# Kernel tuning notes

Measured on AMD Instinct MI355X. Metric: run time of the kernel, lower is better.

The kernel has to match this reference:

```python
import jax, jax.numpy as jnp
import numpy as np
from math import ceil, log2

LEVELS = 8
# pywt 'db4' filters (length 8)
DB4_DEC_HI = np.array([-0.23037781330885523, 0.7148465705525415, -0.6308807679295904,
                       -0.02798376941698385, 0.18703481171888114, 0.030841381835986965,
                       -0.032883011666982945, -0.010597401784997278], dtype=np.float32)
DB4_REC_HI = np.array([-0.010597401784997278, -0.032883011666982945, 0.030841381835986965,
                       0.18703481171888114, -0.02798376941698385, -0.6308807679295904,
                       0.7148465705525415, -0.23037781330885523], dtype=np.float32)


def setup_inputs() -> dict:
    key = jax.random.key(0)
    x = jax.random.normal(key, (2048, 3000), dtype=jnp.float32)
    scaling = jnp.tile(jnp.asarray(DB4_DEC_HI), (LEVELS, 1))       # [levels, 8]
    scaling_rec = jnp.tile(jnp.asarray(DB4_REC_HI), (LEVELS, 1))   # [levels, 8]
    return {"input": x, "scaling": scaling, "scaling_rec": scaling_rec}


def _make_wavelet(h):
    # g = flip(h); g[1::2] *= -1
    g = jnp.flip(h, axis=-1)
    signs = jnp.where(jnp.arange(g.shape[-1]) % 2 == 1, -1.0, 1.0).astype(g.dtype)
    return g * signs


def _circ_conv(x, filt, transpose=False):
    # FFT-based circular convolution (filter zero-padded to input length)
    L = x.shape[-1]
    ra = jnp.fft.rfft(x)
    rb = jnp.fft.rfft(filt, n=L)
    if transpose:
        rb = jnp.conj(rb)
    return jnp.fft.irfft(ra * rb, n=L)


def _upsample2(x):
    # interleave zeros: out[:, ::2] = x
    n, k = x.shape
    out = jnp.zeros((n, 2 * k), dtype=x.dtype)
    return out.at[:, ::2].set(x)


def _forward(x, scaling, scaling_rec):
    levels = scaling.shape[0]
    m = x.shape[1]
    L = 2 ** ceil(log2(m))
    p0 = (L - m) // 2
    p1 = ceil((L - m) / 2)
    x = jnp.pad(x, ((0, 0), (p0, p1)), mode="edge")  # ReplicationPad1d

    approx = x
    wav_coeffs = []
    for lvl in range(levels):
        wavelet = _make_wavelet(scaling_rec[lvl])
        details = _circ_conv(approx, wavelet)[:, ::2]
        approx = _circ_conv(approx, scaling[lvl])[:, ::2]
        wav_coeffs.append(details)
    wav_coeffs.append(approx)

    # (no thresholding: the original forward copies coeffs unmodified)
    filtered = list(wav_coeffs)
    approx = filtered[-1]
    for lvl in reversed(range(levels)):
        details = filtered[lvl]
        wav_syn = _make_wavelet(scaling_rec[lvl])
        d_rec = _circ_conv(_upsample2(details), wav_syn, transpose=True)
        a_rec = _circ_conv(_upsample2(approx), scaling[lvl], transpose=True)
        approx = d_rec + a_rec

    recon = approx[:, p0:m + p1]
    coeffs = jnp.concatenate(wav_coeffs, axis=-1)  # total length == L
    return recon, coeffs


def reference(input, scaling, scaling_rec):
    return _forward(input, scaling, scaling_rec)
```

## Files before the change

kernel.cpp:

```cpp
#include <hip/hip_runtime.h>

#define NROWS 2048
#define MLEN  3000
#define LPAD  4096
#define PAD0  548
#define NLVL  8
#define NT    256

__global__ __launch_bounds__(NT) void despawn_kernel(
    const float* __restrict__ x,
    const float* __restrict__ scaling,
    const float* __restrict__ scaling_rec,
    float* __restrict__ recon_out,
    float* __restrict__ coef_out)
{
    __shared__ float bufA[LPAD];
    __shared__ float bufB[LPAD / 2];
    __shared__ float coef[LPAD];
    __shared__ float fsca[NLVL * 8];
    __shared__ float fwav[NLVL * 8];

    const int tid = threadIdx.x;
    const int row = blockIdx.x;

    if (tid < NLVL * 8) {
        const int lvl = tid >> 3, k = tid & 7;
        fsca[tid] = scaling[tid];
        fwav[tid] = scaling_rec[lvl * 8 + (7 - k)] * ((k & 1) ? -1.0f : 1.0f);
    }

    const float* xr = x + (size_t)row * MLEN;
    for (int i = tid; i < LPAD; i += NT) {
        int j = i - PAD0;
        j = j < 0 ? 0 : (j > MLEN - 1 ? MLEN - 1 : j);
        bufA[i] = xr[j];
    }
    __syncthreads();

    float* cur = bufA;
    float* alt = bufB;
    int   Ml  = LPAD;
    int   coff = 0;
    for (int lvl = 0; lvl < NLVL; ++lvl) {
        const int half = Ml >> 1;
        const int mask = Ml - 1;
        const float* w = &fwav[lvl * 8];
        const float* s = &fsca[lvl * 8];
        for (int j = tid; j < half; j += NT) {
            const int b = 2 * j;
            float ds = 0.0f, as = 0.0f;
#pragma unroll
            for (int k = 0; k < 8; ++k) {
                const float v = cur[(b - k) & mask];
                ds = fmaf(v, w[k], ds);
                as = fmaf(v, s[k], as);
            }
            coef[coff + j] = ds;
            alt[j] = as;
        }
        __syncthreads();
        coff += half;
        float* t = cur; cur = alt; alt = t;
        Ml = half;
    }
    if (tid < 16) coef[LPAD - 16 + tid] = cur[tid];
    __syncthreads();

    const float* a = &coef[LPAD - 16];
    int len = 16;
    float* obuf = bufB;
    for (int lvl = NLVL - 1; lvl >= 0; --lvl) {
        const int Mout  = len << 1;
        const int lmask = len - 1;
        const float* d = &coef[LPAD - (LPAD >> lvl)];
        const float* w = &fwav[lvl * 8];
        const float* s = &fsca[lvl * 8];
        for (int n = tid; n < Mout; n += NT) {
            const int p = n & 1;
            float sum = 0.0f;
#pragma unroll
            for (int t4 = 0; t4 < 4; ++t4) {
                const int k   = p + 2 * t4;
                const int idx = ((n + k) >> 1) & lmask;
                sum = fmaf(d[idx], w[k], sum);
                sum = fmaf(a[idx], s[k], sum);
            }
            obuf[n] = sum;
        }
        __syncthreads();
        a   = obuf;
        len = Mout;
        obuf = (obuf == bufB) ? bufA : bufB;
    }

    float* ro = recon_out + (size_t)row * MLEN;
    for (int i = tid; i < MLEN; i += NT) ro[i] = a[PAD0 + i];

    float* co = coef_out + (size_t)row * LPAD;
    for (int i = tid; i < LPAD; i += NT) co[i] = coef[i];
}

extern "C" void kernel_launch(void* const* d_in, const int* in_sizes, int n_in,
                              void* d_out, int out_size, void* d_ws, size_t ws_size,
                              hipStream_t stream) {
    const float* x           = (const float*)d_in[0];
    const float* scaling     = (const float*)d_in[1];
    const float* scaling_rec = (const float*)d_in[2];
    float* recon = (float*)d_out;
    float* coefo = recon + (size_t)NROWS * MLEN;
    despawn_kernel<<<dim3(NROWS), dim3(NT), 0, stream>>>(x, scaling, scaling_rec,
                                                         recon, coefo);
    (void)in_sizes; (void)n_in; (void)out_size; (void)d_ws; (void)ws_size;
}
```

Measured before the change: 110.9 us.

## Store levels deinterleaved in LDS, keep detail coefficients in global memory, shrink LDS

The signal is kept in LDS split into even and odd halves, so the strided filter taps become contiguous reads and bank conflicts drop. Detail coefficients are written straight to the global output row and read back from there during reconstruction, instead of being staged in a 16 KB shared array. This removes the final LDS-to-global copy and cuts LDS per block from about 40 KB to about 24 KB, which allows more blocks per CU. The cost is that reconstruction reads details from global memory (L2-resident), and it relies on the block's own global writes being visible after __syncthreads.

After: 113.8 us. 2.6% more time.

```diff
diff --git a/kernel.cpp b/kernel.cpp
--- a/kernel.cpp
+++ b/kernel.cpp
@@ -14,14 +14,14 @@
     float* __restrict__ recon_out,
     float* __restrict__ coef_out)
 {
-    __shared__ float bufA[LPAD];
-    __shared__ float bufB[LPAD / 2];
-    __shared__ float coef[LPAD];
+    __shared__ float SA[LPAD];
+    __shared__ float SB[LPAD / 2];
     __shared__ float fsca[NLVL * 8];
     __shared__ float fwav[NLVL * 8];
 
     const int tid = threadIdx.x;
     const int row = blockIdx.x;
+    float* const crow = coef_out + (size_t)row * LPAD;
 
     if (tid < NLVL * 8) {
         const int lvl = tid >> 3, k = tid & 7;
@@ -33,71 +33,76 @@
     for (int i = tid; i < LPAD; i += NT) {
         int j = i - PAD0;
         j = j < 0 ? 0 : (j > MLEN - 1 ? MLEN - 1 : j);
-        bufA[i] = xr[j];
+        SA[((i & 1) ? (LPAD / 2) : 0) + (i >> 1)] = xr[j];
     }
     __syncthreads();
 
-    float* cur = bufA;
-    float* alt = bufB;
-    int   Ml  = LPAD;
-    int   coff = 0;
+    float* cur = SA;
+    float* alt = SB;
+    int M = LPAD;
+    int coff = 0;
     for (int lvl = 0; lvl < NLVL; ++lvl) {
-        const int half = Ml >> 1;
-        const int mask = Ml - 1;
-        const float* w = &fwav[lvl * 8];
-        const float* s = &fsca[lvl * 8];
-        for (int j = tid; j < half; j += NT) {
-            const int b = 2 * j;
+        const int H = M >> 1;
+        const int hm = H - 1;
+        const float* we = &fwav[lvl * 8];
+        const float* se = &fsca[lvl * 8];
+        const float* ev = cur;
+        const float* od = cur + H;
+        for (int j = tid; j < H; j += NT) {
             float ds = 0.0f, as = 0.0f;
 #pragma unroll
-            for (int k = 0; k < 8; ++k) {
-                const float v = cur[(b - k) & mask];
-                ds = fmaf(v, w[k], ds);
-                as = fmaf(v, s[k], as);
+            for (int m = 0; m < 4; ++m) {
+                const float vE = ev[(j - m) & hm];
+                const float vO = od[(j - m - 1) & hm];
+                ds = fmaf(vE, we[2 * m], ds);
+                ds = fmaf(vO, we[2 * m + 1], ds);
+                as = fmaf(vE, se[2 * m], as);
+                as = fmaf(vO, se[2 * m + 1], as);
             }
-            coef[coff + j] = ds;
-            alt[j] = as;
+            crow[coff + j] = ds;
+            alt[((j & 1) ? (H >> 1) : 0) + (j >> 1)] = as;
         }
         __syncthreads();
-        coff += half;
+        coff += H;
         float* t = cur; cur = alt; alt = t;
-        Ml = half;
+        M = H;
     }
-    if (tid < 16) coef[LPAD - 16 + tid] = cur[tid];
+    if (tid < 16) {
+        const float v = cur[((tid & 1) ? 8 : 0) + (tid >> 1)];
+        crow[LPAD - 16 + tid] = v;
+        SA[16 + tid] = v;
+    }
     __syncthreads();
 
-    const float* a = &coef[LPAD - 16];
+    const float* a = SA + 16;
     int len = 16;
-    float* obuf = bufB;
+    float* obuf = SB;
     for (int lvl = NLVL - 1; lvl >= 0; --lvl) {
-        const int Mout  = len << 1;
+        const int Mout = len << 1;
         const int lmask = len - 1;
-        const float* d = &coef[LPAD - (LPAD >> lvl)];
-        const float* w = &fwav[lvl * 8];
-        const float* s = &fsca[lvl * 8];
+        const float* d = crow + (LPAD - (LPAD >> lvl));
+        const float* we = &fwav[lvl * 8];
+        const float* se = &fsca[lvl * 8];
         for (int n = tid; n < Mout; n += NT) {
             const int p = n & 1;
+            const int i0 = (n + p) >> 1;
             float sum = 0.0f;
 #pragma unroll
-            for (int t4 = 0; t4 < 4; ++t4) {
-                const int k   = p + 2 * t4;
-                const int idx = ((n + k) >> 1) & lmask;
-                sum = fmaf(d[idx], w[k], sum);
-                sum = fmaf(a[idx], s[k], sum);
+            for (int m = 0; m < 4; ++m) {
+                const int idx = (i0 + m) & lmask;
+                sum = fmaf(d[idx], we[p + 2 * m], sum);
+                sum = fmaf(a[idx], se[p + 2 * m], sum);
             }
             obuf[n] = sum;
         }
         __syncthreads();
-        a   = obuf;
+        a = obuf;
         len = Mout;
-        obuf = (obuf == bufB) ? bufA : bufB;
+        obuf = (obuf == SB) ? SA : SB;
     }
 
     float* ro = recon_out + (size_t)row * MLEN;
     for (int i = tid; i < MLEN; i += NT) ro[i] = a[PAD0 + i];
-
-    float* co = coef_out + (size_t)row * LPAD;
-    for (int i = tid; i < LPAD; i += NT) co[i] = coef[i];
 }
 
 extern "C" void kernel_launch(void* const* d_in, const int* in_sizes, int n_in,
```
